# Kernel optimization log

Hardware: AMD Instinct MI355X
Metric: run time of the kernel (lower is better)

The kernel has to match this reference:

```python
import jax, jax.numpy as jnp
import numpy as np

B, IN_DIM, HID = 16384, 256, 512
DT, N_STEPS_ARG = 0.1, 1
N_SOLVER_STEPS = 8  # fixed-step dopri5 substitute for adaptive dopri5

# Dormand-Prince (dopri5) tableau (5th-order solution weights)
_A = (
    (1/5,),
    (3/40, 9/40),
    (44/45, -56/15, 32/9),
    (19372/6561, -25360/2187, 64448/6561, -212/729),
    (9017/3168, -355/33, 46732/5247, 49/176, -5103/18656),
)
_B = (35/384, 0.0, 500/1113, 125/192, -2187/6784, 11/84)


def setup_inputs() -> dict:
    key = jax.random.key(0)
    ks = jax.random.split(key, 10)
    s_in = 1.0 / np.sqrt(IN_DIM)
    s_h = 1.0 / np.sqrt(HID)
    return {
        "y": jax.random.normal(ks[0], (B, HID), jnp.float32),
        "u_t": jax.random.normal(ks[1], (B, IN_DIM), jnp.float32),
        "Wp": jax.random.uniform(ks[2], (IN_DIM, HID), jnp.float32, -s_in, s_in),
        "bp": jax.random.uniform(ks[3], (HID,), jnp.float32, -s_in, s_in),
        "W1": jax.random.uniform(ks[4], (HID, HID), jnp.float32, -s_h, s_h),
        "b1": jax.random.uniform(ks[5], (HID,), jnp.float32, -s_h, s_h),
        "W2": jax.random.uniform(ks[6], (HID, HID), jnp.float32, -s_h, s_h),
        "b2": jax.random.uniform(ks[7], (HID,), jnp.float32, -s_h, s_h),
        "W3": jax.random.uniform(ks[8], (HID, HID), jnp.float32, -s_h, s_h),
        "b3": jax.random.uniform(ks[9], (HID,), jnp.float32, -s_h, s_h),
    }


def _ode_f(y, W1, b1, W2, b2, W3, b3):
    h = jnp.tanh(y @ W1 + b1)
    h = jnp.tanh(h @ W2 + b2)
    return h @ W3 + b3


def reference(y, u_t, Wp, bp, W1, b1, W2, b2, W3, b3):
    y0 = y + (u_t @ Wp + bp)  # input projection added to state
    T = DT * N_STEPS_ARG
    h = jnp.asarray(T / N_SOLVER_STEPS, y0.dtype)
    f = lambda s: _ode_f(s, W1, b1, W2, b2, W3, b3)

    def step(s, _):
        k1 = f(s)
        k2 = f(s + h * (_A[0][0] * k1))
        k3 = f(s + h * (_A[1][0] * k1 + _A[1][1] * k2))
        k4 = f(s + h * (_A[2][0] * k1 + _A[2][1] * k2 + _A[2][2] * k3))
        k5 = f(s + h * (_A[3][0] * k1 + _A[3][1] * k2 + _A[3][2] * k3 + _A[3][3] * k4))
        k6 = f(s + h * (_A[4][0] * k1 + _A[4][1] * k2 + _A[4][2] * k3 + _A[4][3] * k4 + _A[4][4] * k5))
        s_next = s + h * (_B[0] * k1 + _B[2] * k3 + _B[3] * k4 + _B[4] * k5 + _B[5] * k6)
        return s_next, None

    y_final, _ = jax.lax.scan(step, y0, None, length=N_SOLVER_STEPS)
    return y_final
```

## Files before the change

kernel.cpp:

```cpp
#include <hip/hip_runtime.h>
#include <hip/hip_bf16.h>
#include <cstddef>

typedef unsigned short u16;
typedef short bf16x8 __attribute__((ext_vector_type(8)));
typedef float f32x4 __attribute__((ext_vector_type(4)));
typedef unsigned short u16x8 __attribute__((ext_vector_type(8)));
typedef unsigned short u16x4 __attribute__((ext_vector_type(4)));

#define MDIM 16384
#define NDIM 512
#define HPAD 520

__device__ __forceinline__ float b2f(u16 u) {
    return __uint_as_float(((unsigned int)u) << 16);
}
__device__ __forceinline__ u16 f2b(float f) {
    unsigned int x = __float_as_uint(f);
    x += 0x7fffu + ((x >> 16) & 1u);
    return (u16)(x >> 16);
}
__device__ __forceinline__ float fast_tanh(float x) {
    float e = __expf(2.0f * x);
    return 1.0f - 2.0f * __builtin_amdgcn_rcpf(e + 1.0f);
}

template <int KDIM, int EPI, bool AF32>
__global__ __launch_bounds__(256, 2) void gemm_bt(
    const void* __restrict__ Avoid, const u16* __restrict__ Bt,
    const float* __restrict__ bias, const float* __restrict__ addf,
    u16* __restrict__ Cb, float* __restrict__ Cf) {
    __shared__ u16 As[128 * 72];
    __shared__ u16 Bs[128 * 72];
    const int tid = threadIdx.x;
    const int m0 = blockIdx.y * 128;
    const int n0 = blockIdx.x * 128;
    const int lane = tid & 63;
    const int wave = tid >> 6;
    const int wm = (wave & 1) * 64;
    const int wn = (wave >> 1) * 64;
    const int lr = lane & 15;
    const int lk = (lane >> 4) * 8;

    f32x4 acc[4][4];
    f32x4 zero = {0.0f, 0.0f, 0.0f, 0.0f};
#pragma unroll
    for (int i = 0; i < 4; ++i)
#pragma unroll
        for (int j = 0; j < 4; ++j) acc[i][j] = zero;

    const int r0 = tid >> 3;
    const int c0 = (tid & 7) * 8;

    for (int kt = 0; kt < KDIM / 64; ++kt) {
        const int k0 = kt * 64;
#pragma unroll
        for (int it = 0; it < 4; ++it) {
            int r = it * 32 + r0;
            if constexpr (AF32) {
                const float* Af = (const float*)Avoid;
                const float* src = Af + (size_t)(m0 + r) * KDIM + k0 + c0;
                f32x4 lo = *(const f32x4*)(src);
                f32x4 hi = *(const f32x4*)(src + 4);
                u16x8 t;
#pragma unroll
                for (int q = 0; q < 4; ++q) { t[q] = f2b(lo[q]); t[q + 4] = f2b(hi[q]); }
                *(u16x8*)(&As[r * 72 + c0]) = t;
            } else {
                const u16* Ab = (const u16*)Avoid;
                *(f32x4*)(&As[r * 72 + c0]) =
                    *(const f32x4*)(Ab + (size_t)(m0 + r) * KDIM + k0 + c0);
            }
            *(f32x4*)(&Bs[r * 72 + c0]) =
                *(const f32x4*)(Bt + (size_t)(n0 + r) * KDIM + k0 + c0);
        }
        __syncthreads();
#pragma unroll
        for (int kk = 0; kk < 2; ++kk) {
            bf16x8 af[4], bw[4];
#pragma unroll
            for (int i = 0; i < 4; ++i) {
                af[i] = __builtin_bit_cast(
                    bf16x8, *(const f32x4*)(&As[(wm + i * 16 + lr) * 72 + kk * 32 + lk]));
                bw[i] = __builtin_bit_cast(
                    bf16x8, *(const f32x4*)(&Bs[(wn + i * 16 + lr) * 72 + kk * 32 + lk]));
            }
#pragma unroll
            for (int i = 0; i < 4; ++i)
#pragma unroll
                for (int j = 0; j < 4; ++j)
                    acc[i][j] = __builtin_amdgcn_mfma_f32_16x16x32_bf16(
                        af[i], bw[j], acc[i][j], 0, 0, 0);
        }
        __syncthreads();
    }
#pragma unroll
    for (int j = 0; j < 4; ++j) {
        const int col = n0 + wn + j * 16 + lr;
        const float bv = bias[col];
#pragma unroll
        for (int i = 0; i < 4; ++i) {
            const int rowb = m0 + wm + i * 16 + (lane >> 4) * 4;
#pragma unroll
            for (int r = 0; r < 4; ++r) {
                float v = acc[i][j][r] + bv;
                size_t off = (size_t)(rowb + r) * NDIM + col;
                if constexpr (EPI == 2) Cb[off] = f2b(v);
                if constexpr (EPI == 3) {
                    v += addf[off];
                    Cf[off] = v;
                }
            }
        }
    }
}

__device__ __forceinline__ void k_load(const u16* __restrict__ G, size_t kbase,
                                       u16x4 (&g)[4][4]) {
#pragma unroll
    for (int i = 0; i < 4; ++i)
#pragma unroll
        for (int j = 0; j < 4; ++j)
            g[i][j] = *(const u16x4*)(G + kbase + (size_t)(i * 4 + j) * 2048);
}

__global__ __launch_bounds__(512, 2) void ode_mega(
    const float* __restrict__ S32,
    const u16* __restrict__ W1t, const float* __restrict__ bb1,
    const u16* __restrict__ W2t, const float* __restrict__ bb2,
    const u16* __restrict__ W3t, const float* __restrict__ bb3,
    u16* __restrict__ G1, u16* __restrict__ G2,
    u16* __restrict__ G3, u16* __restrict__ G4,
    float* __restrict__ OUT) {
    __shared__ u16 As[64 * HPAD];
    __shared__ u16 Hs[64 * HPAD];
    const int tid = threadIdx.x;
    const int lane = tid & 63;
    const int wn = (tid >> 6) * 64;
    const int lr = lane & 15;
    const int lq = lane >> 4;
    const int lk = lq * 8;
    const size_t row0 = (size_t)blockIdx.x * 64;
    const size_t kbase = (size_t)blockIdx.x * (16 * 512 * 4) + (size_t)tid * 4;

    constexpr double h = 0.1 / 8.0;
    constexpr float A21 = (float)(h * 1.0 / 5.0);
    constexpr float A31 = (float)(h * 3.0 / 40.0), A32 = (float)(h * 9.0 / 40.0);
    constexpr float A41 = (float)(h * 44.0 / 45.0), A42 = (float)(h * -56.0 / 15.0);
    constexpr float A43 = (float)(h * 32.0 / 9.0);
    constexpr float A51 = (float)(h * 19372.0 / 6561.0), A52 = (float)(h * -25360.0 / 2187.0);
    constexpr float A53 = (float)(h * 64448.0 / 6561.0), A54 = (float)(h * -212.0 / 729.0);
    constexpr float A61 = (float)(h * 9017.0 / 3168.0), A62 = (float)(h * -355.0 / 33.0);
    constexpr float A63 = (float)(h * 46732.0 / 5247.0), A64 = (float)(h * 49.0 / 176.0);
    constexpr float A65 = (float)(h * -5103.0 / 18656.0);
    constexpr float B1c = (float)(h * 35.0 / 384.0), B3c = (float)(h * 500.0 / 1113.0);
    constexpr float B4c = (float)(h * 125.0 / 192.0), B5c = (float)(h * -2187.0 / 6784.0);
    constexpr float B6c = (float)(h * 11.0 / 84.0);

    const f32x4 zf = {0.f, 0.f, 0.f, 0.f};
    f32x4 S[4][4];
#pragma unroll
    for (int i = 0; i < 4; ++i)
#pragma unroll
        for (int j = 0; j < 4; ++j) {
#pragma unroll
            for (int r = 0; r < 4; ++r)
                S[i][j][r] = S32[(row0 + i * 16 + lq * 4 + r) * 512 + wn + j * 16 + lr];
        }

    u16x4 kA[4][4], kB[4][4];
    f32x4 acc[4][4];

#define STAGE_STORE(sv, i, j)                                                      \
    do {                                                                           \
        const int col_ = wn + (j) * 16 + lr;                                       \
        const int rw_ = (i) * 16 + lq * 4;                                         \
        As[(rw_ + 0) * HPAD + col_] = f2b(sv[0]);                                  \
        As[(rw_ + 1) * HPAD + col_] = f2b(sv[1]);                                  \
        As[(rw_ + 2) * HPAD + col_] = f2b(sv[2]);                                  \
        As[(rw_ + 3) * HPAD + col_] = f2b(sv[3]);                                  \
    } while (0)

#define STG_BEGIN                                                                  \
    _Pragma("unroll") for (int i = 0; i < 4; ++i)                                  \
    _Pragma("unroll") for (int j = 0; j < 4; ++j) {                                \
        f32x4 sv = S[i][j];

#define ADDT(c, K)                                                                 \
        {                                                                          \
            u16x4 t_ = (K)[i][j];                                                  \
            _Pragma("unroll") for (int r_ = 0; r_ < 4; ++r_)                       \
                sv[r_] += (c) * b2f(t_[r_]);                                       \
        }

#define STG_END                                                                    \
        STAGE_STORE(sv, i, j);                                                     \
    }

#define LAYER(SRC, WT)                                                             \
    do {                                                                           \
        _Pragma("unroll") for (int i_ = 0; i_ < 4; ++i_)                           \
            _Pragma("unroll") for (int j_ = 0; j_ < 4; ++j_) acc[i_][j_] = zf;     \
        _Pragma("unroll 2") for (int kt = 0; kt < 16; ++kt) {                      \
            bf16x8 af[4], bw[4];                                                   \
            _Pragma("unroll") for (int j_ = 0; j_ < 4; ++j_)                       \
                bw[j_] = __builtin_bit_cast(bf16x8,                                \
                    *(const f32x4*)(WT + (size_t)((wn + j_ * 16 + lr) << 9) +      \
                                    kt * 32 + lk));                                \
            _Pragma("unroll") for (int i_ = 0; i_ < 4; ++i_)                       \
                af[i_] = __builtin_bit_cast(bf16x8,                                \
                    *(const f32x4*)(&SRC[(i_ * 16 + lr) * HPAD + kt * 32 + lk]));  \
            _Pragma("unroll") for (int i_ = 0; i_ < 4; ++i_)                       \
                _Pragma("unroll") for (int j_ = 0; j_ < 4; ++j_)                   \
                    acc[i_][j_] = __builtin_amdgcn_mfma_f32_16x16x32_bf16(         \
                        af[i_], bw[j_], acc[i_][j_], 0, 0, 0);                     \
        }                                                                          \
    } while (0)

#define EPI_TANH(BIAS, DST)                                                        \
    do {                                                                           \
        _Pragma("unroll") for (int j_ = 0; j_ < 4; ++j_) {                         \
            const float bv = BIAS[wn + j_ * 16 + lr];                              \
            _Pragma("unroll") for (int i_ = 0; i_ < 4; ++i_) {                     \
                const int rb = i_ * 16 + lq * 4;                                   \
                _Pragma("unroll") for (int r_ = 0; r_ < 4; ++r_)                   \
                    DST[(rb + r_) * HPAD + wn + j_ * 16 + lr] =                    \
                        f2b(fast_tanh(acc[i_][j_][r_] + bv));                      \
            }                                                                      \
        }                                                                          \
    } while (0)

#define EPI_K(KD, GP)                                                              \
    do {                                                                           \
        _Pragma("unroll") for (int j_ = 0; j_ < 4; ++j_) {                         \
            const float bv = bb3[wn + j_ * 16 + lr];                               \
            _Pragma("unroll") for (int i_ = 0; i_ < 4; ++i_) {                     \
                u16x4 kv_;                                                         \
                _Pragma("unroll") for (int r_ = 0; r_ < 4; ++r_)                   \
                    kv_[r_] = f2b(acc[i_][j_][r_] + bv);                           \
                KD[i_][j_] = kv_;                                                  \
                if ((GP) != nullptr)                                               \
                    *(u16x4*)((u16*)(GP) + kbase + (size_t)(i_ * 4 + j_) * 2048) = \
                        kv_;                                                       \
            }                                                                      \
        }                                                                          \
    } while (0)

#define MLP3(KD, GP)                                                               \
    do {                                                                           \
        LAYER(As, W1t);                                                            \
        EPI_TANH(bb1, Hs);                                                         \
        __syncthreads();                                                           \
        LAYER(Hs, W2t);                                                            \
        EPI_TANH(bb2, As);                                                         \
        __syncthreads();                                                           \
        LAYER(As, W3t);                                                            \
        __syncthreads();                                                           \
        EPI_K(KD, GP);                                                             \
    } while (0)

#pragma clang loop unroll(disable)
    for (int st = 0; st < 8; ++st) {
        STG_BEGIN STG_END
        __syncthreads();
        MLP3(kA, G1);

        STG_BEGIN ADDT(A21, kA) STG_END
        __syncthreads();
        MLP3(kB, G2);

        STG_BEGIN ADDT(A31, kA) ADDT(A32, kB) STG_END
        __syncthreads();
        MLP3(kA, G3);

        {
            u16x4 g1[4][4];
            k_load(G1, kbase, g1);
            STG_BEGIN ADDT(A41, g1) ADDT(A42, kB) ADDT(A43, kA) STG_END
        }
        __syncthreads();
        MLP3(kB, G4);

        {
            u16x4 g1[4][4], g2[4][4];
            k_load(G1, kbase, g1);
            k_load(G2, kbase, g2);
            STG_BEGIN ADDT(A51, g1) ADDT(A52, g2) ADDT(A53, kA) ADDT(A54, kB) STG_END
        }
        __syncthreads();
        MLP3(kA, (u16*)nullptr);

        {
            u16x4 g1[4][4], g2[4][4], g3[4][4];
            k_load(G1, kbase, g1);
            k_load(G2, kbase, g2);
            k_load(G3, kbase, g3);
            STG_BEGIN ADDT(A61, g1) ADDT(A62, g2) ADDT(A63, g3) ADDT(A64, kB)
                ADDT(A65, kA) STG_END
        }
        __syncthreads();
        MLP3(kB, (u16*)nullptr);

        {
            u16x4 g1[4][4], g3[4][4], g4[4][4];
            k_load(G1, kbase, g1);
            k_load(G3, kbase, g3);
            k_load(G4, kbase, g4);
            const bool last = (st == 7);
#pragma unroll
            for (int i = 0; i < 4; ++i)
#pragma unroll
                for (int j = 0; j < 4; ++j) {
                    u16x4 t1 = g1[i][j], t3 = g3[i][j], t4 = g4[i][j];
                    u16x4 t5 = kA[i][j], t6 = kB[i][j];
#pragma unroll
                    for (int r = 0; r < 4; ++r)
                        S[i][j][r] += B1c * b2f(t1[r]) + B3c * b2f(t3[r]) +
                                      B4c * b2f(t4[r]) + B5c * b2f(t5[r]) +
                                      B6c * b2f(t6[r]);
                    if (last) {
                        const int col = wn + j * 16 + lr;
                        const int rw = i * 16 + lq * 4;
#pragma unroll
                        for (int r = 0; r < 4; ++r)
                            OUT[(row0 + rw + r) * 512 + col] = S[i][j][r];
                    }
                }
        }
    }
#undef MLP3
#undef EPI_K
#undef EPI_TANH
#undef LAYER
#undef STG_END
#undef ADDT
#undef STG_BEGIN
#undef STAGE_STORE
}

__global__ void transpose_k(const float* __restrict__ in, u16* __restrict__ out,
                            int R, int Ncols) {
    int idx = blockIdx.x * 256 + threadIdx.x;
    int r = idx / Ncols, c = idx % Ncols;
    out[(size_t)c * R + r] = f2b(in[idx]);
}

extern "C" void kernel_launch(void* const* d_in, const int* in_sizes, int n_in,
                              void* d_out, int out_size, void* d_ws, size_t ws_size,
                              hipStream_t stream) {
    const float *y = nullptr, *u_t = nullptr, *Wp = nullptr, *bp = nullptr;
    const float *W1 = nullptr, *b1 = nullptr, *W2 = nullptr, *b2 = nullptr;
    const float *W3 = nullptr, *b3 = nullptr;
    {
        const float* w262[3] = {nullptr, nullptr, nullptr};
        const float* s512[4] = {nullptr, nullptr, nullptr, nullptr};
        int i512[4] = {0, 0, 0, 0};
        int n262 = 0, n512 = 0;
        for (int i = 0; i < n_in; ++i) {
            const float* p = (const float*)d_in[i];
            int sz = in_sizes[i];
            if (sz == MDIM * NDIM) y = p;
            else if (sz == MDIM * 256) u_t = p;
            else if (sz == 256 * 512) Wp = p;
            else if (sz == 512 * 512) { if (n262 < 3) w262[n262++] = p; }
            else if (sz == 512) { if (n512 < 4) { i512[n512] = i; s512[n512++] = p; } }
        }
        W1 = w262[0]; W2 = w262[1]; W3 = w262[2];
        bool contig = (n512 == 4) && (i512[3] == i512[0] + 3);
        if (contig) { b1 = s512[0]; b2 = s512[1]; b3 = s512[2]; bp = s512[3]; }
        else        { bp = s512[0]; b1 = s512[1]; b2 = s512[2]; b3 = s512[3]; }
        if (!y || !u_t || !Wp || !W1 || n512 < 4) {
            y  = (const float*)d_in[0]; u_t = (const float*)d_in[1];
            Wp = (const float*)d_in[2]; bp  = (const float*)d_in[3];
            W1 = (const float*)d_in[4]; b1  = (const float*)d_in[5];
            W2 = (const float*)d_in[6]; b2  = (const float*)d_in[7];
            W3 = (const float*)d_in[8]; b3  = (const float*)d_in[9];
        }
    }

    u16* ws  = (u16*)d_ws;
    u16* Wpt = ws;
    u16* W1t = Wpt + 512 * 256;
    u16* W2t = W1t + 512 * 512;
    u16* W3t = W2t + 512 * 512;
    const size_t wfix = 512 * 256 + 3 * 512 * 512;

    long wsElems = (long)(ws_size / 2);
    long chunk = (wsElems - (long)wfix) / (6L * NDIM);
    chunk = (chunk / 128) * 128;
    if (chunk > MDIM) chunk = MDIM;
    if (chunk < 128) chunk = 128;

    transpose_k<<<512, 256, 0, stream>>>(Wp, Wpt, 256, 512);
    transpose_k<<<1024, 256, 0, stream>>>(W1, W1t, 512, 512);
    transpose_k<<<1024, 256, 0, stream>>>(W2, W2t, 512, 512);
    transpose_k<<<1024, 256, 0, stream>>>(W3, W3t, 512, 512);

    float* OUT = (float*)d_out;

    for (long row0 = 0; row0 < MDIM; row0 += chunk) {
        const long rows = (MDIM - row0 < chunk) ? (MDIM - row0) : chunk;
        const size_t CB = (size_t)rows * NDIM;

        u16* base = ws + wfix;
        float* S32 = (float*)base;
        u16* G1 = base + 2 * CB;
        u16* G2 = base + 3 * CB;
        u16* G3 = base + 4 * CB;
        u16* G4 = base + 5 * CB;

        dim3 gg(4, (unsigned)(rows / 128));
        gemm_bt<256, 3, true><<<gg, 256, 0, stream>>>(
            (const void*)(u_t + (size_t)row0 * 256), Wpt, bp,
            y + (size_t)row0 * NDIM, nullptr, S32);

        const int nb = (int)(rows / 64);
        ode_mega<<<nb, 512, 0, stream>>>(
            S32, W1t, b1, W2t, b2, W3t, b3,
            G1, G2, G3, G4,
            OUT + (size_t)row0 * NDIM);
    }
}
```

Before: 3.417 ms.

## Cut register-held stage buffers, spill k5 to global, vectorize k loads/stores

Only one register-resident stage result (kA) is kept instead of two. k5 is written to a fifth global scratch buffer, and the final solution update is folded into the next step's first stage. Scratch loads and stores become 16-byte per-thread contiguous chunks processed in pairs of fragments, which reduces register pressure and widens memory accesses. The occupancy hint of 2 in launch_bounds is dropped. In exchange there is extra global traffic for k5 and larger workspace needs, which can shrink chunk size.

```diff
diff --git a/kernel.cpp b/kernel.cpp
--- a/kernel.cpp
+++ b/kernel.cpp
@@ -115,22 +115,13 @@
     }
 }
 
-__device__ __forceinline__ void k_load(const u16* __restrict__ G, size_t kbase,
-                                       u16x4 (&g)[4][4]) {
-#pragma unroll
-    for (int i = 0; i < 4; ++i)
-#pragma unroll
-        for (int j = 0; j < 4; ++j)
-            g[i][j] = *(const u16x4*)(G + kbase + (size_t)(i * 4 + j) * 2048);
-}
-
-__global__ __launch_bounds__(512, 2) void ode_mega(
+__global__ __launch_bounds__(512) void ode_mega(
     const float* __restrict__ S32,
     const u16* __restrict__ W1t, const float* __restrict__ bb1,
     const u16* __restrict__ W2t, const float* __restrict__ bb2,
     const u16* __restrict__ W3t, const float* __restrict__ bb3,
-    u16* __restrict__ G1, u16* __restrict__ G2,
-    u16* __restrict__ G3, u16* __restrict__ G4,
+    u16* __restrict__ G1, u16* __restrict__ G2, u16* __restrict__ G3,
+    u16* __restrict__ G4, u16* __restrict__ G5,
     float* __restrict__ OUT) {
     __shared__ u16 As[64 * HPAD];
     __shared__ u16 Hs[64 * HPAD];
@@ -141,7 +132,7 @@
     const int lq = lane >> 4;
     const int lk = lq * 8;
     const size_t row0 = (size_t)blockIdx.x * 64;
-    const size_t kbase = (size_t)blockIdx.x * (16 * 512 * 4) + (size_t)tid * 4;
+    const size_t kb64 = (size_t)blockIdx.x * 32768 + (size_t)tid * 64;
 
     constexpr double h = 0.1 / 8.0;
     constexpr float A21 = (float)(h * 1.0 / 5.0);
@@ -168,34 +159,40 @@
                 S[i][j][r] = S32[(row0 + i * 16 + lq * 4 + r) * 512 + wn + j * 16 + lr];
         }
 
-    u16x4 kA[4][4], kB[4][4];
+    u16x4 kA[4][4];
     f32x4 acc[4][4];
 
-#define STAGE_STORE(sv, i, j)                                                      \
+#define STAGE(NG, UKA, PERSIST, P0, P1, P2, P3, C0, C1, C2, C3, CKA)               \
     do {                                                                           \
-        const int col_ = wn + (j) * 16 + lr;                                       \
-        const int rw_ = (i) * 16 + lq * 4;                                         \
-        As[(rw_ + 0) * HPAD + col_] = f2b(sv[0]);                                  \
-        As[(rw_ + 1) * HPAD + col_] = f2b(sv[1]);                                  \
-        As[(rw_ + 2) * HPAD + col_] = f2b(sv[2]);                                  \
-        As[(rw_ + 3) * HPAD + col_] = f2b(sv[3]);                                  \
+        _Pragma("unroll 2") for (int fg = 0; fg < 8; ++fg) {                       \
+            u16x8 gv0, gv1, gv2, gv3;                                              \
+            if (NG >= 1) gv0 = *(const u16x8*)((P0) + kb64 + fg * 8);              \
+            if (NG >= 2) gv1 = *(const u16x8*)((P1) + kb64 + fg * 8);              \
+            if (NG >= 3) gv2 = *(const u16x8*)((P2) + kb64 + fg * 8);              \
+            if (NG >= 4) gv3 = *(const u16x8*)((P3) + kb64 + fg * 8);              \
+            _Pragma("unroll") for (int hf = 0; hf < 2; ++hf) {                     \
+                const int f_ = fg * 2 + hf;                                        \
+                const int i_ = f_ >> 2, j_ = f_ & 3;                               \
+                f32x4 sv = S[i_][j_];                                              \
+                _Pragma("unroll") for (int r_ = 0; r_ < 4; ++r_) {                 \
+                    float a_ = sv[r_];                                             \
+                    if (NG >= 1) a_ += (C0) * b2f(gv0[hf * 4 + r_]);               \
+                    if (NG >= 2) a_ += (C1) * b2f(gv1[hf * 4 + r_]);               \
+                    if (NG >= 3) a_ += (C2) * b2f(gv2[hf * 4 + r_]);               \
+                    if (NG >= 4) a_ += (C3) * b2f(gv3[hf * 4 + r_]);               \
+                    if (UKA) a_ += (CKA) * b2f(kA[i_][j_][r_]);                    \
+                    sv[r_] = a_;                                                   \
+                }                                                                  \
+                if (PERSIST) S[i_][j_] = sv;                                       \
+                const int col_ = wn + j_ * 16 + lr;                                \
+                const int rw_ = i_ * 16 + lq * 4;                                  \
+                As[(rw_ + 0) * HPAD + col_] = f2b(sv[0]);                          \
+                As[(rw_ + 1) * HPAD + col_] = f2b(sv[1]);                          \
+                As[(rw_ + 2) * HPAD + col_] = f2b(sv[2]);                          \
+                As[(rw_ + 3) * HPAD + col_] = f2b(sv[3]);                          \
+            }                                                                      \
+        }                                                                          \
     } while (0)
-
-#define STG_BEGIN                                                                  \
-    _Pragma("unroll") for (int i = 0; i < 4; ++i)                                  \
-    _Pragma("unroll") for (int j = 0; j < 4; ++j) {                                \
-        f32x4 sv = S[i][j];
-
-#define ADDT(c, K)                                                                 \
-        {                                                                          \
-            u16x4 t_ = (K)[i][j];                                                  \
-            _Pragma("unroll") for (int r_ = 0; r_ < 4; ++r_)                       \
-                sv[r_] += (c) * b2f(t_[r_]);                                       \
-        }
-
-#define STG_END                                                                    \
-        STAGE_STORE(sv, i, j);                                                     \
-    }
 
 #define LAYER(SRC, WT)                                                             \
     do {                                                                           \
@@ -230,24 +227,34 @@
         }                                                                          \
     } while (0)
 
-#define EPI_K(KD, GP)                                                              \
+#define EPI_K(GP)                                                                  \
     do {                                                                           \
         _Pragma("unroll") for (int j_ = 0; j_ < 4; ++j_) {                         \
             const float bv = bb3[wn + j_ * 16 + lr];                               \
             _Pragma("unroll") for (int i_ = 0; i_ < 4; ++i_) {                     \
-                u16x4 kv_;                                                         \
+                u16x4 kv;                                                          \
                 _Pragma("unroll") for (int r_ = 0; r_ < 4; ++r_)                   \
-                    kv_[r_] = f2b(acc[i_][j_][r_] + bv);                           \
-                KD[i_][j_] = kv_;                                                  \
-                if ((GP) != nullptr)                                               \
-                    *(u16x4*)((u16*)(GP) + kbase + (size_t)(i_ * 4 + j_) * 2048) = \
-                        kv_;                                                       \
+                    kv[r_] = f2b(acc[i_][j_][r_] + bv);                            \
+                kA[i_][j_] = kv;                                                   \
+            }                                                                      \
+        }                                                                          \
+        if ((GP) != nullptr) {                                                     \
+            _Pragma("unroll") for (int fg = 0; fg < 8; ++fg) {                     \
+                const int f0 = fg * 2;                                             \
+                const int i_ = f0 >> 2, j0 = f0 & 3;                               \
+                u16x8 w;                                                           \
+                _Pragma("unroll") for (int r_ = 0; r_ < 4; ++r_) {                 \
+                    w[r_] = kA[i_][j0][r_];                                        \
+                    w[r_ + 4] = kA[i_][j0 + 1][r_];                                \
+                }                                                                  \
+                *(u16x8*)((u16*)(GP) + kb64 + fg * 8) = w;                         \
             }                                                                      \
         }                                                                          \
     } while (0)
 
-#define MLP3(KD, GP)                                                               \
+#define MLP3(GP)                                                                   \
     do {                                                                           \
+        __syncthreads();                                                           \
         LAYER(As, W1t);                                                            \
         EPI_TANH(bb1, Hs);                                                         \
         __syncthreads();                                                           \
@@ -256,86 +263,59 @@
         __syncthreads();                                                           \
         LAYER(As, W3t);                                                            \
         __syncthreads();                                                           \
-        EPI_K(KD, GP);                                                             \
+        EPI_K(GP);                                                                 \
     } while (0)
 
 #pragma clang loop unroll(disable)
     for (int st = 0; st < 8; ++st) {
-        STG_BEGIN STG_END
-        __syncthreads();
-        MLP3(kA, G1);
-
-        STG_BEGIN ADDT(A21, kA) STG_END
-        __syncthreads();
-        MLP3(kB, G2);
-
-        STG_BEGIN ADDT(A31, kA) ADDT(A32, kB) STG_END
-        __syncthreads();
-        MLP3(kA, G3);
-
-        {
-            u16x4 g1[4][4];
-            k_load(G1, kbase, g1);
-            STG_BEGIN ADDT(A41, g1) ADDT(A42, kB) ADDT(A43, kA) STG_END
-        }
-        __syncthreads();
-        MLP3(kB, G4);
-
-        {
-            u16x4 g1[4][4], g2[4][4];
-            k_load(G1, kbase, g1);
-            k_load(G2, kbase, g2);
-            STG_BEGIN ADDT(A51, g1) ADDT(A52, g2) ADDT(A53, kA) ADDT(A54, kB) STG_END
-        }
-        __syncthreads();
-        MLP3(kA, (u16*)nullptr);
-
-        {
-            u16x4 g1[4][4], g2[4][4], g3[4][4];
-            k_load(G1, kbase, g1);
-            k_load(G2, kbase, g2);
-            k_load(G3, kbase, g3);
-            STG_BEGIN ADDT(A61, g1) ADDT(A62, g2) ADDT(A63, g3) ADDT(A64, kB)
-                ADDT(A65, kA) STG_END
-        }
-        __syncthreads();
-        MLP3(kB, (u16*)nullptr);
-
-        {
-            u16x4 g1[4][4], g3[4][4], g4[4][4];
-            k_load(G1, kbase, g1);
-            k_load(G3, kbase, g3);
-            k_load(G4, kbase, g4);
-            const bool last = (st == 7);
-#pragma unroll
-            for (int i = 0; i < 4; ++i)
-#pragma unroll
-                for (int j = 0; j < 4; ++j) {
-                    u16x4 t1 = g1[i][j], t3 = g3[i][j], t4 = g4[i][j];
-                    u16x4 t5 = kA[i][j], t6 = kB[i][j];
-#pragma unroll
-                    for (int r = 0; r < 4; ++r)
-                        S[i][j][r] += B1c * b2f(t1[r]) + B3c * b2f(t3[r]) +
-                                      B4c * b2f(t4[r]) + B5c * b2f(t5[r]) +
-                                      B6c * b2f(t6[r]);
-                    if (last) {
-                        const int col = wn + j * 16 + lr;
-                        const int rw = i * 16 + lq * 4;
-#pragma unroll
-                        for (int r = 0; r < 4; ++r)
-                            OUT[(row0 + rw + r) * 512 + col] = S[i][j][r];
-                    }
-                }
+        if (st == 0)
+            STAGE(0, 0, 0, G1, G1, G1, G1, 0.f, 0.f, 0.f, 0.f, 0.f);
+        else
+            STAGE(4, 1, 1, G1, G3, G4, G5, B1c, B3c, B4c, B5c, B6c);
+        MLP3(G1);
+
+        STAGE(0, 1, 0, G1, G1, G1, G1, 0.f, 0.f, 0.f, 0.f, A21);
+        MLP3(G2);
+
+        STAGE(1, 1, 0, G1, G1, G1, G1, A31, 0.f, 0.f, 0.f, A32);
+        MLP3(G3);
+
+        STAGE(2, 1, 0, G1, G2, G2, G2, A41, A42, 0.f, 0.f, A43);
+        MLP3(G4);
+
+        STAGE(3, 1, 0, G1, G2, G3, G3, A51, A52, A53, 0.f, A54);
+        MLP3(G5);
+
+        STAGE(4, 1, 0, G1, G2, G3, G4, A61, A62, A63, A64, A65);
+        MLP3((u16*)nullptr);
+    }
+
+#pragma unroll 2
+    for (int fg = 0; fg < 8; ++fg) {
+        u16x8 g1v = *(const u16x8*)(G1 + kb64 + fg * 8);
+        u16x8 g3v = *(const u16x8*)(G3 + kb64 + fg * 8);
+        u16x8 g4v = *(const u16x8*)(G4 + kb64 + fg * 8);
+        u16x8 g5v = *(const u16x8*)(G5 + kb64 + fg * 8);
+#pragma unroll
+        for (int hf = 0; hf < 2; ++hf) {
+            const int f = fg * 2 + hf;
+            const int i = f >> 2, j = f & 3;
+            const int col = wn + j * 16 + lr;
+            const int rw = i * 16 + lq * 4;
+#pragma unroll
+            for (int r = 0; r < 4; ++r) {
+                float v = S[i][j][r] + B1c * b2f(g1v[hf * 4 + r]) +
+                          B3c * b2f(g3v[hf * 4 + r]) + B4c * b2f(g4v[hf * 4 + r]) +
+                          B5c * b2f(g5v[hf * 4 + r]) + B6c * b2f(kA[i][j][r]);
+                OUT[(row0 + rw + r) * 512 + col] = v;
+            }
         }
     }
 #undef MLP3
 #undef EPI_K
 #undef EPI_TANH
 #undef LAYER
-#undef STG_END
-#undef ADDT
-#undef STG_BEGIN
-#undef STAGE_STORE
+#undef STAGE
 }
 
 __global__ void transpose_k(const float* __restrict__ in, u16* __restrict__ out,
@@ -386,7 +366,7 @@
     const size_t wfix = 512 * 256 + 3 * 512 * 512;
 
     long wsElems = (long)(ws_size / 2);
-    long chunk = (wsElems - (long)wfix) / (6L * NDIM);
+    long chunk = (wsElems - (long)wfix) / (7L * NDIM);
     chunk = (chunk / 128) * 128;
     if (chunk > MDIM) chunk = MDIM;
     if (chunk < 128) chunk = 128;
@@ -408,6 +388,7 @@
         u16* G2 = base + 3 * CB;
         u16* G3 = base + 4 * CB;
         u16* G4 = base + 5 * CB;
+        u16* G5 = base + 6 * CB;
 
         dim3 gg(4, (unsigned)(rows / 128));
         gemm_bt<256, 3, true><<<gg, 256, 0, stream>>>(
@@ -417,7 +398,7 @@
         const int nb = (int)(rows / 64);
         ode_mega<<<nb, 512, 0, stream>>>(
             S32, W1t, b1, W2t, b2, W3t, b3,
-            G1, G2, G3, G4,
+            G1, G2, G3, G4, G5,
             OUT + (size_t)row0 * NDIM);
     }
 }
```

After: 5.530 ms. 1.62x slower.
